# Performance work log

Hardware: AMD Instinct MI355X
Metric: run time of the kernel (lower is better)

## Reference

```python
import jax, jax.numpy as jnp
import numpy as np

N_NODES = 100_000
N_EDGES = 1_200_000
N_GRAPHS = 512
HID = 64


def setup_inputs() -> dict:
    key = jax.random.key(0)
    ks = jax.random.split(key, 8)
    x = jax.random.normal(ks[0], (N_NODES, 2), dtype=jnp.float32)
    edge_index = jax.random.randint(ks[1], (2, N_EDGES), 0, N_NODES, dtype=jnp.int32)
    batch = jnp.sort(jax.random.randint(ks[2], (N_NODES,), 0, N_GRAPHS, dtype=jnp.int32))
    def glorot(k, shape):
        fan_in, fan_out = shape
        s = jnp.sqrt(6.0 / (fan_in + fan_out))
        return jax.random.uniform(k, shape, jnp.float32, -s, s)
    return {
        "x": x, "edge_index": edge_index, "batch": batch, "num_graphs": N_GRAPHS,
        "W1": glorot(ks[3], (2, HID)), "b1": jnp.zeros((HID,), jnp.float32),
        "W2": glorot(ks[4], (HID, HID)), "b2": jnp.zeros((HID,), jnp.float32),
        "Wf1": glorot(ks[5], (HID, HID)), "bf1": jnp.zeros((HID,), jnp.float32),
        "Wf2": glorot(ks[6], (HID, 4)), "bf2": jnp.zeros((4,), jnp.float32),
    }


def gcn_conv(x, W, b, src, dst, n_nodes):
    """PyG GCNConv: sym-normalized A with self-loops, then linear."""
    h = x @ W  # [N, H] transform first (as PyG does)
    ones = jnp.ones(src.shape[0], x.dtype)
    deg = jax.ops.segment_sum(ones, dst, num_segments=n_nodes) + 1.0  # +1 self-loop
    dinv = jax.lax.rsqrt(deg)  # deg >= 1 always
    norm = dinv[src] * dinv[dst]  # [E]
    agg = jax.ops.segment_sum(h[src] * norm[:, None], dst, num_segments=n_nodes)
    agg = agg + h * (dinv * dinv)[:, None]  # self-loop contribution
    return agg + b


def global_mean_pool(x, batch, num_graphs):
    sums = jax.ops.segment_sum(x, batch, num_segments=num_graphs)
    cnts = jax.ops.segment_sum(jnp.ones(x.shape[0], x.dtype), batch, num_segments=num_graphs)
    return sums / jnp.maximum(cnts, 1.0)[:, None]


def reference(x, edge_index, batch, num_graphs, W1, b1, W2, b2, Wf1, bf1, Wf2, bf2):
    n = x.shape[0]
    src, dst = edge_index[0], edge_index[1]
    h = jax.nn.relu(gcn_conv(x, W1, b1, src, dst, n))   # dropout = identity (eval)
    h = jax.nn.relu(gcn_conv(h, W2, b2, src, dst, n))
    g = global_mean_pool(h, batch, num_graphs)          # [num_graphs, HID]
    g = jax.nn.relu(g @ Wf1 + bf1)
    return g @ Wf2 + bf2                                # [num_graphs, 4]
```

## Files before the change

### kernel.cpp

```cpp
#include <hip/hip_runtime.h>

#define NG 512
#define HID 64
#define CSH 9
#define BKT (1 << CSH)
#define PTILE 4096
#define MAXB 1024

__device__ __forceinline__ int pad8(int d) { return (d + 7) & ~7; }

__global__ __launch_bounds__(256) void chist_kernel(const int* __restrict__ dst,
                                                    int* __restrict__ chist, int E, int nbc) {
    __shared__ int h[MAXB];
    for (int i = threadIdx.x; i < nbc; i += 256) h[i] = 0;
    __syncthreads();
    int t0 = blockIdx.x * PTILE;
#pragma unroll
    for (int j = 0; j < PTILE / 256; ++j) {
        int e = t0 + j * 256 + threadIdx.x;
        if (e < E) atomicAdd(&h[dst[e] >> CSH], 1);
    }
    __syncthreads();
    for (int i = threadIdx.x; i < nbc; i += 256)
        if (h[i]) atomicAdd(&chist[i], h[i]);
}

__global__ __launch_bounds__(1024) void cscan_kernel(const int* __restrict__ chist,
                                                     int* __restrict__ cofs,
                                                     int* __restrict__ ccur, int nbc, int E) {
    __shared__ int s[1024];
    int i = threadIdx.x;
    int v = (i < nbc) ? chist[i] : 0;
    s[i] = v;
    __syncthreads();
    for (int off = 1; off < 1024; off <<= 1) {
        int t = (i >= off) ? s[i - off] : 0;
        __syncthreads();
        s[i] += t;
        __syncthreads();
    }
    if (i < nbc) {
        int ex = s[i] - v;
        cofs[i] = ex;
        ccur[i] = ex;
    }
    if (i == 0) cofs[nbc] = E;
}

__global__ __launch_bounds__(1024) void bscan_kernel(const int* __restrict__ bsum,
                                                     int* __restrict__ bofs, int nbc) {
    __shared__ int s[1024];
    int i = threadIdx.x;
    int v = (i < nbc) ? bsum[i] : 0;
    s[i] = v;
    __syncthreads();
    for (int off = 1; off < 1024; off <<= 1) {
        int t = (i >= off) ? s[i - off] : 0;
        __syncthreads();
        s[i] += t;
        __syncthreads();
    }
    if (i < nbc) bofs[i] = s[i] - v;
}

__global__ __launch_bounds__(256) void partA_kernel(const int* __restrict__ src,
                                                    const int* __restrict__ dst,
                                                    int* __restrict__ ccur,
                                                    int2* __restrict__ pstage, int E, int nbc) {
    __shared__ int hist[MAXB];
    __shared__ int base[MAXB];
    int tid = threadIdx.x;
    int t0 = blockIdx.x * PTILE;
    for (int i = tid; i < nbc; i += 256) hist[i] = 0;
    __syncthreads();
    int es[PTILE / 256], ds[PTILE / 256];
#pragma unroll
    for (int j = 0; j < PTILE / 256; ++j) {
        int e = t0 + j * 256 + tid;
        if (e < E) {
            ds[j] = dst[e];
            es[j] = src[e];
            atomicAdd(&hist[ds[j] >> CSH], 1);
        } else {
            ds[j] = -1;
        }
    }
    __syncthreads();
    for (int i = tid; i < nbc; i += 256) {
        int c = hist[i];
        base[i] = c ? atomicAdd(&ccur[i], c) : 0;
        hist[i] = 0;
    }
    __syncthreads();
#pragma unroll
    for (int j = 0; j < PTILE / 256; ++j) {
        if (ds[j] >= 0) {
            int b = ds[j] >> CSH;
            int r = atomicAdd(&hist[b], 1);
            pstage[base[b] + r] = make_int2(es[j], ds[j]);
        }
    }
}

__global__ __launch_bounds__(256) void degB_kernel(const int2* __restrict__ pstage,
                                                   const int* __restrict__ cofs,
                                                   const float2* __restrict__ x2,
                                                   int* __restrict__ deg,
                                                   float* __restrict__ dinv,
                                                   float2* __restrict__ xs2,
                                                   int* __restrict__ bsum, int N) {
    __shared__ int h[BKT];
    __shared__ int rs[256];
    int c = blockIdx.x;
    int n0 = c << CSH;
    int tid = threadIdx.x;
    for (int i = tid; i < BKT; i += 256) h[i] = 0;
    __syncthreads();
    int s0 = cofs[c], s1 = cofs[c + 1];
    for (int i = s0 + tid; i < s1; i += 256) atomicAdd(&h[pstage[i].y - n0], 1);
    __syncthreads();
    int psum = 0;
    for (int l = tid; l < BKT; l += 256) {
        int d = n0 + l;
        if (d < N) {
            int dg = h[l];
            deg[d] = dg;
            float di = rsqrtf((float)dg + 1.0f);
            dinv[d] = di;
            float2 xv = x2[d];
            xs2[d] = make_float2(xv.x * di, xv.y * di);
            psum += pad8(dg);
        }
    }
    rs[tid] = psum;
    __syncthreads();
    for (int off = 128; off > 0; off >>= 1) {
        if (tid < off) rs[tid] += rs[tid + off];
        __syncthreads();
    }
    if (tid == 0) bsum[c] = rs[0];
    if (c == 0 && tid == 0) xs2[N] = make_float2(0.0f, 0.0f);
}

__global__ __launch_bounds__(256) void partB_kernel(const int2* __restrict__ pstage,
                                                    const int* __restrict__ cofs,
                                                    const int* __restrict__ bofs,
                                                    const int* __restrict__ deg,
                                                    int* __restrict__ rowptr,
                                                    int* __restrict__ esrc, int N, int nbc) {
    __shared__ int rowL[BKT];
    __shared__ int curL[BKT];
    __shared__ int ps[256];
    int c = blockIdx.x;
    int n0 = c << CSH;
    int tid = threadIdx.x;
    int i0 = 2 * tid, i1 = 2 * tid + 1;
    int d0 = (n0 + i0 < N) ? pad8(deg[n0 + i0]) : 0;
    int d1 = (n0 + i1 < N) ? pad8(deg[n0 + i1]) : 0;
    ps[tid] = d0 + d1;
    __syncthreads();
    for (int off = 1; off < 256; off <<= 1) {
        int t = (tid >= off) ? ps[tid - off] : 0;
        __syncthreads();
        ps[tid] += t;
        __syncthreads();
    }
    int base = bofs[c];
    int excl = ps[tid] - (d0 + d1);
    rowL[i0] = base + excl;
    rowL[i1] = base + excl + d0;
    curL[i0] = 0;
    curL[i1] = 0;
    if (n0 + i0 < N) rowptr[n0 + i0] = rowL[i0];
    if (n0 + i1 < N) rowptr[n0 + i1] = rowL[i1];
    if (c == nbc - 1 && tid == 255) rowptr[N] = base + ps[255];
    __syncthreads();
    int s0 = cofs[c], s1 = cofs[c + 1];
    for (int i = s0 + tid; i < s1; i += 256) {
        int2 pr = pstage[i];
        int l = pr.y - n0;
        int p = rowL[l] + atomicAdd(&curL[l], 1);
        esrc[p] = pr.x;
    }
    __syncthreads();
    for (int l = tid; l < BKT; l += 256) {
        if (n0 + l < N) {
            int dg = curL[l];
            int p = rowL[l] + dg, p1 = rowL[l] + pad8(dg);
            for (; p < p1; ++p) esrc[p] = N;
        }
    }
}

__global__ void gstart_kernel(const int* __restrict__ batch, int* __restrict__ gstart, int N) {
    int i = blockIdx.x * blockDim.x + threadIdx.x;
    if (i >= N) return;
    int b = batch[i];
    int bp = (i == 0) ? -1 : batch[i - 1];
    for (int g = bp + 1; g <= b; ++g) gstart[g] = i;
    if (i == N - 1)
        for (int g = b + 1; g <= NG; ++g) gstart[g] = N;
}

__global__ __launch_bounds__(256) void layer1a_kernel(
    const float2* __restrict__ xs2, const int* __restrict__ rowptr,
    const int* __restrict__ esrc, const float* __restrict__ dinv,
    const float* __restrict__ W1, const float* __restrict__ b1,
    float* __restrict__ h1s, int N) {
    int t = blockIdx.x * blockDim.x + threadIdx.x;
    int node = t >> 6, lane = t & 63;
    if (node >= N) return;
    int un = __builtin_amdgcn_readfirstlane(node);
    int k0 = __builtin_amdgcn_readfirstlane(rowptr[un]);
    int k1 = __builtin_amdgcn_readfirstlane(rowptr[un + 1]);
    float a0 = 0.0f, a1 = 0.0f;
    for (int e = k0; e < k1; e += 8) {
        const int4* ep = (const int4*)(esrc + e);
        int4 qa = ep[0], qb = ep[1];
        float2 v0 = xs2[qa.x], v1 = xs2[qa.y], v2 = xs2[qa.z], v3 = xs2[qa.w];
        float2 v4 = xs2[qb.x], v5 = xs2[qb.y], v6 = xs2[qb.z], v7 = xs2[qb.w];
        a0 += ((v0.x + v1.x) + (v2.x + v3.x)) + ((v4.x + v5.x) + (v6.x + v7.x));
        a1 += ((v0.y + v1.y) + (v2.y + v3.y)) + ((v4.y + v5.y) + (v6.y + v7.y));
    }
    float di = dinv[un];
    float2 xn = xs2[un];
    float m0 = di * (a0 + xn.x);
    float m1 = di * (a1 + xn.y);
    float v = fmaf(m0, W1[lane], fmaf(m1, W1[HID + lane], b1[lane]));
    h1s[(size_t)un * HID + lane] = fmaxf(v, 0.0f) * di;
}

#define TNB 128
__global__ __launch_bounds__(TNB) void l1gemm_kernel(
    const float* __restrict__ h1s, const float* __restrict__ W2,
    float* __restrict__ h2, int N) {
    __shared__ float h1t[HID * TNB];
    int t = threadIdx.x;
    int node0 = blockIdx.x * TNB;
    const float4* g4 = (const float4*)h1s;
#pragma unroll
    for (int r = 0; r < 16; ++r) {
        int g = r * TNB + t;
        int nd = g >> 4, kq = g & 15;
        float4 v = make_float4(0.f, 0.f, 0.f, 0.f);
        if (node0 + nd < N) v = g4[(size_t)(node0 + nd) * 16 + kq];
        int kb = kq * 4;
        h1t[(kb + 0) * TNB + (nd ^ ((kb + 0) & 31))] = v.x;
        h1t[(kb + 1) * TNB + (nd ^ ((kb + 1) & 31))] = v.y;
        h1t[(kb + 2) * TNB + (nd ^ ((kb + 2) & 31))] = v.z;
        h1t[(kb + 3) * TNB + (nd ^ ((kb + 3) & 31))] = v.w;
    }
    __syncthreads();
    int node = node0 + t;
    bool alive = node < N;
#pragma unroll 1
    for (int jt = 0; jt < 8; ++jt) {
        float c0 = 0.f, c1 = 0.f, c2 = 0.f, c3 = 0.f;
        float c4 = 0.f, c5 = 0.f, c6 = 0.f, c7 = 0.f;
#pragma unroll 8
        for (int k = 0; k < HID; ++k) {
            float h = h1t[k * TNB + (t ^ (k & 31))];
            const float4* wr = (const float4*)(W2 + k * HID + jt * 8);
            float4 wa = wr[0], wb = wr[1];
            c0 = fmaf(h, wa.x, c0); c1 = fmaf(h, wa.y, c1);
            c2 = fmaf(h, wa.z, c2); c3 = fmaf(h, wa.w, c3);
            c4 = fmaf(h, wb.x, c4); c5 = fmaf(h, wb.y, c5);
            c6 = fmaf(h, wb.z, c6); c7 = fmaf(h, wb.w, c7);
        }
        if (alive) {
            float4* o = (float4*)(h2 + (size_t)node * HID + jt * 8);
            o[0] = make_float4(c0, c1, c2, c3);
            o[1] = make_float4(c4, c5, c6, c7);
        }
    }
}

__global__ __launch_bounds__(256, 8) void layer2_kernel(
    const int* __restrict__ rowptr, const int* __restrict__ esrc,
    const float* __restrict__ dinv, const float* __restrict__ h2,
    const float* __restrict__ b2, const int* __restrict__ batch,
    float* __restrict__ gsum, int N) {
    int lane = threadIdx.x & 63;
    float bz = b2[lane];
    int wave = (blockIdx.x * 256 + threadIdx.x) >> 6;
    int nwaves = gridDim.x * 4;
    int npw = (N + nwaves - 1) / nwaves;
    int nA = wave * npw;
    int nB = min(N, nA + npw);
    int gcur = -1;
    float zacc = 0.0f;
    for (int node = nA; node < nB; ++node) {
        int un = __builtin_amdgcn_readfirstlane(node);
        int k0 = __builtin_amdgcn_readfirstlane(rowptr[un]);
        int k1 = __builtin_amdgcn_readfirstlane(rowptr[un + 1]);
        float acc = h2[(un << 6) + lane];
        int e = k0;
        for (; e + 32 <= k1; e += 32) {
            const int4* ep = (const int4*)(esrc + e);
            int4 q0 = ep[0], q1 = ep[1], q2 = ep[2], q3 = ep[3];
            int4 q4 = ep[4], q5 = ep[5], q6 = ep[6], q7 = ep[7];
            float r0  = h2[(q0.x << 6) + lane], r1  = h2[(q0.y << 6) + lane];
            float r2  = h2[(q0.z << 6) + lane], r3  = h2[(q0.w << 6) + lane];
            float r4  = h2[(q1.x << 6) + lane], r5  = h2[(q1.y << 6) + lane];
            float r6  = h2[(q1.z << 6) + lane], r7  = h2[(q1.w << 6) + lane];
            float r8  = h2[(q2.x << 6) + lane], r9  = h2[(q2.y << 6) + lane];
            float r10 = h2[(q2.z << 6) + lane], r11 = h2[(q2.w << 6) + lane];
            float r12 = h2[(q3.x << 6) + lane], r13 = h2[(q3.y << 6) + lane];
            float r14 = h2[(q3.z << 6) + lane], r15 = h2[(q3.w << 6) + lane];
            float r16 = h2[(q4.x << 6) + lane], r17 = h2[(q4.y << 6) + lane];
            float r18 = h2[(q4.z << 6) + lane], r19 = h2[(q4.w << 6) + lane];
            float r20 = h2[(q5.x << 6) + lane], r21 = h2[(q5.y << 6) + lane];
            float r22 = h2[(q5.z << 6) + lane], r23 = h2[(q5.w << 6) + lane];
            float r24 = h2[(q6.x << 6) + lane], r25 = h2[(q6.y << 6) + lane];
            float r26 = h2[(q6.z << 6) + lane], r27 = h2[(q6.w << 6) + lane];
            float r28 = h2[(q7.x << 6) + lane], r29 = h2[(q7.y << 6) + lane];
            float r30 = h2[(q7.z << 6) + lane], r31 = h2[(q7.w << 6) + lane];
            acc += ((((r0 + r1) + (r2 + r3)) + ((r4 + r5) + (r6 + r7)))
                  + (((r8 + r9) + (r10 + r11)) + ((r12 + r13) + (r14 + r15))))
                 + ((((r16 + r17) + (r18 + r19)) + ((r20 + r21) + (r22 + r23)))
                  + (((r24 + r25) + (r26 + r27)) + ((r28 + r29) + (r30 + r31))));
        }
        if (e + 16 <= k1) {
            const int4* ep = (const int4*)(esrc + e);
            int4 qa = ep[0], qb = ep[1], qc = ep[2], qd = ep[3];
            float r0 = h2[(qa.x << 6) + lane], r1 = h2[(qa.y << 6) + lane];
            float r2 = h2[(qa.z << 6) + lane], r3 = h2[(qa.w << 6) + lane];
            float r4 = h2[(qb.x << 6) + lane], r5 = h2[(qb.y << 6) + lane];
            float r6 = h2[(qb.z << 6) + lane], r7 = h2[(qb.w << 6) + lane];
            float r8 = h2[(qc.x << 6) + lane], r9 = h2[(qc.y << 6) + lane];
            float r10 = h2[(qc.z << 6) + lane], r11 = h2[(qc.w << 6) + lane];
            float r12 = h2[(qd.x << 6) + lane], r13 = h2[(qd.y << 6) + lane];
            float r14 = h2[(qd.z << 6) + lane], r15 = h2[(qd.w << 6) + lane];
            acc += (((r0 + r1) + (r2 + r3)) + ((r4 + r5) + (r6 + r7)))
                 + (((r8 + r9) + (r10 + r11)) + ((r12 + r13) + (r14 + r15)));
            e += 16;
        }
        if (e < k1) {
            const int4* ep = (const int4*)(esrc + e);
            int4 qa = ep[0], qb = ep[1];
            float r0 = h2[(qa.x << 6) + lane], r1 = h2[(qa.y << 6) + lane];
            float r2 = h2[(qa.z << 6) + lane], r3 = h2[(qa.w << 6) + lane];
            float r4 = h2[(qb.x << 6) + lane], r5 = h2[(qb.y << 6) + lane];
            float r6 = h2[(qb.z << 6) + lane], r7 = h2[(qb.w << 6) + lane];
            acc += ((r0 + r1) + (r2 + r3)) + ((r4 + r5) + (r6 + r7));
        }
        float z = fmaxf(fmaf(dinv[un], acc, bz), 0.0f);
        int g = __builtin_amdgcn_readfirstlane(batch[un]);
        if (g != gcur) {
            if (gcur >= 0) atomicAdd(&gsum[(gcur << 6) + lane], zacc);
            gcur = g;
            zacc = 0.0f;
        }
        zacc += z;
    }
    if (gcur >= 0) atomicAdd(&gsum[(gcur << 6) + lane], zacc);
}

__global__ void head_kernel(const float* __restrict__ gsum, const int* __restrict__ gstart,
                            const float* __restrict__ Wf1, const float* __restrict__ bf1,
                            const float* __restrict__ Wf2, const float* __restrict__ bf2,
                            float* __restrict__ out) {
    __shared__ float gs[HID];
    __shared__ float ts[HID];
    int b = blockIdx.x;
    int j = threadIdx.x;
    float cnt = fmaxf((float)(gstart[b + 1] - gstart[b]), 1.0f);
    gs[j] = gsum[b * HID + j] / cnt;
    __syncthreads();
    float acc = bf1[j];
#pragma unroll
    for (int k = 0; k < HID; ++k) acc = fmaf(gs[k], Wf1[k * HID + j], acc);
    ts[j] = fmaxf(acc, 0.0f);
    __syncthreads();
    if (j < 4) {
        float o = bf2[j];
#pragma unroll
        for (int k = 0; k < HID; ++k) o = fmaf(ts[k], Wf2[k * 4 + j], o);
        out[b * 4 + j] = o;
    }
}

extern "C" void kernel_launch(void* const* d_in, const int* in_sizes, int n_in,
                              void* d_out, int out_size, void* d_ws, size_t ws_size,
                              hipStream_t stream) {
    const float* x   = (const float*)d_in[0];
    const int*   ei  = (const int*)d_in[1];
    const int*   bat = (const int*)d_in[2];
    const float* W1  = (const float*)d_in[4];
    const float* b1  = (const float*)d_in[5];
    const float* W2  = (const float*)d_in[6];
    const float* b2  = (const float*)d_in[7];
    const float* Wf1 = (const float*)d_in[8];
    const float* bf1 = (const float*)d_in[9];
    const float* Wf2 = (const float*)d_in[10];
    const float* bf2 = (const float*)d_in[11];
    float* out = (float*)d_out;

    int N = in_sizes[2];
    int E = in_sizes[1] / 2;
    const int* src = ei;
    const int* dst = ei + E;
    int nbc = (N + BKT - 1) >> CSH;
    int ntile = (E + PTILE - 1) / PTILE;
    size_t Ecap = ((size_t)E + 7 * (size_t)N + 8 + 3) & ~(size_t)3;

    char* ws = (char*)d_ws;
    size_t off = 0;
    auto alloc = [&](size_t bytes) {
        char* p = ws + off;
        off = (off + bytes + 255) & ~(size_t)255;
        return p;
    };
    int*    chist  = (int*)alloc((size_t)MAXB * 4);
    float*  gsum   = (float*)alloc((size_t)NG * HID * 4);
    int*    deg    = (int*)alloc((size_t)N * 4);
    int*    cofs   = (int*)alloc((size_t)(MAXB + 1) * 4);
    int*    ccur   = (int*)alloc((size_t)MAXB * 4);
    float*  dinv   = (float*)alloc((size_t)N * 4);
    int*    rowptr = (int*)alloc((size_t)(N + 1) * 4);
    int*    bsum   = (int*)alloc((size_t)MAXB * 4);
    int*    bofs   = (int*)alloc((size_t)MAXB * 4);
    int*    esrc   = (int*)alloc(Ecap * 4);
    int2*   pstage = (int2*)alloc((size_t)E * 8);
    float2* xs2    = (float2*)alloc((size_t)(N + 1) * 8);
    float*  h1buf  = (float*)alloc((size_t)N * HID * 4);
    float*  h2buf  = (float*)alloc((size_t)(N + 1) * HID * 4);
    int*    gstart = (int*)alloc((size_t)(NG + 1) * 4);

    hipMemsetAsync(chist, 0, (size_t)((char*)gsum - (char*)chist) + (size_t)NG * HID * 4,
                   stream);
    hipMemsetAsync(h2buf + (size_t)N * HID, 0, HID * 4, stream);

    chist_kernel<<<ntile, 256, 0, stream>>>(dst, chist, E, nbc);
    gstart_kernel<<<(N + 255) / 256, 256, 0, stream>>>(bat, gstart, N);
    cscan_kernel<<<1, 1024, 0, stream>>>(chist, cofs, ccur, nbc, E);
    partA_kernel<<<ntile, 256, 0, stream>>>(src, dst, ccur, pstage, E, nbc);
    degB_kernel<<<nbc, 256, 0, stream>>>(pstage, cofs, (const float2*)x, deg, dinv, xs2,
                                         bsum, N);
    bscan_kernel<<<1, 1024, 0, stream>>>(bsum, bofs, nbc);
    partB_kernel<<<nbc, 256, 0, stream>>>(pstage, cofs, bofs, deg, rowptr, esrc, N, nbc);

    int nh = N * HID;
    layer1a_kernel<<<(nh + 255) / 256, 256, 0, stream>>>(xs2, rowptr, esrc, dinv, W1, b1,
                                                         h1buf, N);
    l1gemm_kernel<<<(N + TNB - 1) / TNB, TNB, 0, stream>>>(h1buf, W2, h2buf, N);

    layer2_kernel<<<4096, 256, 0, stream>>>(rowptr, esrc, dinv, h2buf, b2, bat, gsum, N);

    head_kernel<<<NG, HID, 0, stream>>>(gsum, gstart, Wf1, bf1, Wf2, bf2, out);
}
```

Baseline: 261.8 us.

## Fuse degree and CSR fill kernels and store layer-2 features in fp16

Merges degB, bscan and partB into one kernel. Each bucket block now claims its CSR segment with an atomicAdd on a global cursor instead of a separate global scan, so rows are stored as rowbeg plus degree rather than a contiguous rowptr. Separately, the transformed layer-2 features are written as fp16, which halves the bytes fetched by the irregular gather in layer2 while accumulation stays in fp32. The fp16 storage loses precision, and the atomic segment allocation makes edge placement order nondeterministic across blocks.

```diff
diff --git a/kernel.cpp b/kernel.cpp
--- a/kernel.cpp
+++ b/kernel.cpp
@@ -1,4 +1,5 @@
 #include <hip/hip_runtime.h>
+#include <hip/hip_fp16.h>
 
 #define NG 512
 #define HID 64
@@ -45,22 +46,6 @@
         ccur[i] = ex;
     }
     if (i == 0) cofs[nbc] = E;
-}
-
-__global__ __launch_bounds__(1024) void bscan_kernel(const int* __restrict__ bsum,
-                                                     int* __restrict__ bofs, int nbc) {
-    __shared__ int s[1024];
-    int i = threadIdx.x;
-    int v = (i < nbc) ? bsum[i] : 0;
-    s[i] = v;
-    __syncthreads();
-    for (int off = 1; off < 1024; off <<= 1) {
-        int t = (i >= off) ? s[i - off] : 0;
-        __syncthreads();
-        s[i] += t;
-        __syncthreads();
-    }
-    if (i < nbc) bofs[i] = s[i] - v;
 }
 
 __global__ __launch_bounds__(256) void partA_kernel(const int* __restrict__ src,
@@ -102,15 +87,16 @@
     }
 }
 
-__global__ __launch_bounds__(256) void degB_kernel(const int2* __restrict__ pstage,
-                                                   const int* __restrict__ cofs,
-                                                   const float2* __restrict__ x2,
-                                                   int* __restrict__ deg,
-                                                   float* __restrict__ dinv,
-                                                   float2* __restrict__ xs2,
-                                                   int* __restrict__ bsum, int N) {
+__global__ __launch_bounds__(256) void partB2_kernel(
+    const int2* __restrict__ pstage, const int* __restrict__ cofs,
+    const float2* __restrict__ x2, int* __restrict__ deg, float* __restrict__ dinv,
+    float2* __restrict__ xs2, int* __restrict__ rowbeg, int* __restrict__ esrc,
+    int* __restrict__ ecur, int N) {
     __shared__ int h[BKT];
-    __shared__ int rs[256];
+    __shared__ int rowL[BKT];
+    __shared__ int curL[BKT];
+    __shared__ int ps[256];
+    __shared__ int baseS;
     int c = blockIdx.x;
     int n0 = c << CSH;
     int tid = threadIdx.x;
@@ -119,45 +105,25 @@
     int s0 = cofs[c], s1 = cofs[c + 1];
     for (int i = s0 + tid; i < s1; i += 256) atomicAdd(&h[pstage[i].y - n0], 1);
     __syncthreads();
-    int psum = 0;
-    for (int l = tid; l < BKT; l += 256) {
-        int d = n0 + l;
-        if (d < N) {
-            int dg = h[l];
-            deg[d] = dg;
-            float di = rsqrtf((float)dg + 1.0f);
-            dinv[d] = di;
-            float2 xv = x2[d];
-            xs2[d] = make_float2(xv.x * di, xv.y * di);
-            psum += pad8(dg);
-        }
-    }
-    rs[tid] = psum;
-    __syncthreads();
-    for (int off = 128; off > 0; off >>= 1) {
-        if (tid < off) rs[tid] += rs[tid + off];
-        __syncthreads();
-    }
-    if (tid == 0) bsum[c] = rs[0];
-    if (c == 0 && tid == 0) xs2[N] = make_float2(0.0f, 0.0f);
-}
-
-__global__ __launch_bounds__(256) void partB_kernel(const int2* __restrict__ pstage,
-                                                    const int* __restrict__ cofs,
-                                                    const int* __restrict__ bofs,
-                                                    const int* __restrict__ deg,
-                                                    int* __restrict__ rowptr,
-                                                    int* __restrict__ esrc, int N, int nbc) {
-    __shared__ int rowL[BKT];
-    __shared__ int curL[BKT];
-    __shared__ int ps[256];
-    int c = blockIdx.x;
-    int n0 = c << CSH;
-    int tid = threadIdx.x;
     int i0 = 2 * tid, i1 = 2 * tid + 1;
-    int d0 = (n0 + i0 < N) ? pad8(deg[n0 + i0]) : 0;
-    int d1 = (n0 + i1 < N) ? pad8(deg[n0 + i1]) : 0;
-    ps[tid] = d0 + d1;
+    int dg0 = (n0 + i0 < N) ? h[i0] : 0;
+    int dg1 = (n0 + i1 < N) ? h[i1] : 0;
+    if (n0 + i0 < N) {
+        deg[n0 + i0] = dg0;
+        float di = rsqrtf((float)dg0 + 1.0f);
+        dinv[n0 + i0] = di;
+        float2 xv = x2[n0 + i0];
+        xs2[n0 + i0] = make_float2(xv.x * di, xv.y * di);
+    }
+    if (n0 + i1 < N) {
+        deg[n0 + i1] = dg1;
+        float di = rsqrtf((float)dg1 + 1.0f);
+        dinv[n0 + i1] = di;
+        float2 xv = x2[n0 + i1];
+        xs2[n0 + i1] = make_float2(xv.x * di, xv.y * di);
+    }
+    int p0 = pad8(dg0), p1 = pad8(dg1);
+    ps[tid] = p0 + p1;
     __syncthreads();
     for (int off = 1; off < 256; off <<= 1) {
         int t = (tid >= off) ? ps[tid - off] : 0;
@@ -165,17 +131,16 @@
         ps[tid] += t;
         __syncthreads();
     }
-    int base = bofs[c];
-    int excl = ps[tid] - (d0 + d1);
-    rowL[i0] = base + excl;
-    rowL[i1] = base + excl + d0;
+    if (tid == 255) baseS = atomicAdd(ecur, ps[255]);
+    __syncthreads();
+    int excl = baseS + ps[tid] - (p0 + p1);
+    rowL[i0] = excl;
+    rowL[i1] = excl + p0;
     curL[i0] = 0;
     curL[i1] = 0;
-    if (n0 + i0 < N) rowptr[n0 + i0] = rowL[i0];
-    if (n0 + i1 < N) rowptr[n0 + i1] = rowL[i1];
-    if (c == nbc - 1 && tid == 255) rowptr[N] = base + ps[255];
-    __syncthreads();
-    int s0 = cofs[c], s1 = cofs[c + 1];
+    if (n0 + i0 < N) rowbeg[n0 + i0] = rowL[i0];
+    if (n0 + i1 < N) rowbeg[n0 + i1] = rowL[i1];
+    __syncthreads();
     for (int i = s0 + tid; i < s1; i += 256) {
         int2 pr = pstage[i];
         int l = pr.y - n0;
@@ -186,10 +151,11 @@
     for (int l = tid; l < BKT; l += 256) {
         if (n0 + l < N) {
             int dg = curL[l];
-            int p = rowL[l] + dg, p1 = rowL[l] + pad8(dg);
-            for (; p < p1; ++p) esrc[p] = N;
-        }
-    }
+            int p = rowL[l] + dg, p1e = rowL[l] + pad8(dg);
+            for (; p < p1e; ++p) esrc[p] = N;
+        }
+    }
+    if (c == 0 && tid == 0) xs2[N] = make_float2(0.0f, 0.0f);
 }
 
 __global__ void gstart_kernel(const int* __restrict__ batch, int* __restrict__ gstart, int N) {
@@ -203,16 +169,16 @@
 }
 
 __global__ __launch_bounds__(256) void layer1a_kernel(
-    const float2* __restrict__ xs2, const int* __restrict__ rowptr,
-    const int* __restrict__ esrc, const float* __restrict__ dinv,
-    const float* __restrict__ W1, const float* __restrict__ b1,
-    float* __restrict__ h1s, int N) {
+    const float2* __restrict__ xs2, const int* __restrict__ rowbeg,
+    const int* __restrict__ deg, const int* __restrict__ esrc,
+    const float* __restrict__ dinv, const float* __restrict__ W1,
+    const float* __restrict__ b1, float* __restrict__ h1s, int N) {
     int t = blockIdx.x * blockDim.x + threadIdx.x;
     int node = t >> 6, lane = t & 63;
     if (node >= N) return;
     int un = __builtin_amdgcn_readfirstlane(node);
-    int k0 = __builtin_amdgcn_readfirstlane(rowptr[un]);
-    int k1 = __builtin_amdgcn_readfirstlane(rowptr[un + 1]);
+    int k0 = __builtin_amdgcn_readfirstlane(rowbeg[un]);
+    int k1 = k0 + pad8(__builtin_amdgcn_readfirstlane(deg[un]));
     float a0 = 0.0f, a1 = 0.0f;
     for (int e = k0; e < k1; e += 8) {
         const int4* ep = (const int4*)(esrc + e);
@@ -233,7 +199,7 @@
 #define TNB 128
 __global__ __launch_bounds__(TNB) void l1gemm_kernel(
     const float* __restrict__ h1s, const float* __restrict__ W2,
-    float* __restrict__ h2, int N) {
+    __half* __restrict__ h2, int N) {
     __shared__ float h1t[HID * TNB];
     int t = threadIdx.x;
     int node0 = blockIdx.x * TNB;
@@ -268,18 +234,21 @@
             c6 = fmaf(h, wb.z, c6); c7 = fmaf(h, wb.w, c7);
         }
         if (alive) {
-            float4* o = (float4*)(h2 + (size_t)node * HID + jt * 8);
-            o[0] = make_float4(c0, c1, c2, c3);
-            o[1] = make_float4(c4, c5, c6, c7);
+            union { __half h[8]; int4 v; } u;
+            u.h[0] = __float2half_rn(c0); u.h[1] = __float2half_rn(c1);
+            u.h[2] = __float2half_rn(c2); u.h[3] = __float2half_rn(c3);
+            u.h[4] = __float2half_rn(c4); u.h[5] = __float2half_rn(c5);
+            u.h[6] = __float2half_rn(c6); u.h[7] = __float2half_rn(c7);
+            *(int4*)(h2 + (size_t)node * HID + jt * 8) = u.v;
         }
     }
 }
 
 __global__ __launch_bounds__(256, 8) void layer2_kernel(
-    const int* __restrict__ rowptr, const int* __restrict__ esrc,
-    const float* __restrict__ dinv, const float* __restrict__ h2,
-    const float* __restrict__ b2, const int* __restrict__ batch,
-    float* __restrict__ gsum, int N) {
+    const int* __restrict__ rowbeg, const int* __restrict__ deg,
+    const int* __restrict__ esrc, const float* __restrict__ dinv,
+    const __half* __restrict__ h2, const float* __restrict__ b2,
+    const int* __restrict__ batch, float* __restrict__ gsum, int N) {
     int lane = threadIdx.x & 63;
     float bz = b2[lane];
     int wave = (blockIdx.x * 256 + threadIdx.x) >> 6;
@@ -291,30 +260,46 @@
     float zacc = 0.0f;
     for (int node = nA; node < nB; ++node) {
         int un = __builtin_amdgcn_readfirstlane(node);
-        int k0 = __builtin_amdgcn_readfirstlane(rowptr[un]);
-        int k1 = __builtin_amdgcn_readfirstlane(rowptr[un + 1]);
-        float acc = h2[(un << 6) + lane];
+        int k0 = __builtin_amdgcn_readfirstlane(rowbeg[un]);
+        int k1 = k0 + pad8(__builtin_amdgcn_readfirstlane(deg[un]));
+        float acc = __half2float(h2[(un << 6) + lane]);
         int e = k0;
         for (; e + 32 <= k1; e += 32) {
             const int4* ep = (const int4*)(esrc + e);
             int4 q0 = ep[0], q1 = ep[1], q2 = ep[2], q3 = ep[3];
             int4 q4 = ep[4], q5 = ep[5], q6 = ep[6], q7 = ep[7];
-            float r0  = h2[(q0.x << 6) + lane], r1  = h2[(q0.y << 6) + lane];
-            float r2  = h2[(q0.z << 6) + lane], r3  = h2[(q0.w << 6) + lane];
-            float r4  = h2[(q1.x << 6) + lane], r5  = h2[(q1.y << 6) + lane];
-            float r6  = h2[(q1.z << 6) + lane], r7  = h2[(q1.w << 6) + lane];
-            float r8  = h2[(q2.x << 6) + lane], r9  = h2[(q2.y << 6) + lane];
-            float r10 = h2[(q2.z << 6) + lane], r11 = h2[(q2.w << 6) + lane];
-            float r12 = h2[(q3.x << 6) + lane], r13 = h2[(q3.y << 6) + lane];
-            float r14 = h2[(q3.z << 6) + lane], r15 = h2[(q3.w << 6) + lane];
-            float r16 = h2[(q4.x << 6) + lane], r17 = h2[(q4.y << 6) + lane];
-            float r18 = h2[(q4.z << 6) + lane], r19 = h2[(q4.w << 6) + lane];
-            float r20 = h2[(q5.x << 6) + lane], r21 = h2[(q5.y << 6) + lane];
-            float r22 = h2[(q5.z << 6) + lane], r23 = h2[(q5.w << 6) + lane];
-            float r24 = h2[(q6.x << 6) + lane], r25 = h2[(q6.y << 6) + lane];
-            float r26 = h2[(q6.z << 6) + lane], r27 = h2[(q6.w << 6) + lane];
-            float r28 = h2[(q7.x << 6) + lane], r29 = h2[(q7.y << 6) + lane];
-            float r30 = h2[(q7.z << 6) + lane], r31 = h2[(q7.w << 6) + lane];
+            float r0  = __half2float(h2[(q0.x << 6) + lane]);
+            float r1  = __half2float(h2[(q0.y << 6) + lane]);
+            float r2  = __half2float(h2[(q0.z << 6) + lane]);
+            float r3  = __half2float(h2[(q0.w << 6) + lane]);
+            float r4  = __half2float(h2[(q1.x << 6) + lane]);
+            float r5  = __half2float(h2[(q1.y << 6) + lane]);
+            float r6  = __half2float(h2[(q1.z << 6) + lane]);
+            float r7  = __half2float(h2[(q1.w << 6) + lane]);
+            float r8  = __half2float(h2[(q2.x << 6) + lane]);
+            float r9  = __half2float(h2[(q2.y << 6) + lane]);
+            float r10 = __half2float(h2[(q2.z << 6) + lane]);
+            float r11 = __half2float(h2[(q2.w << 6) + lane]);
+            float r12 = __half2float(h2[(q3.x << 6) + lane]);
+            float r13 = __half2float(h2[(q3.y << 6) + lane]);
+            float r14 = __half2float(h2[(q3.z << 6) + lane]);
+            float r15 = __half2float(h2[(q3.w << 6) + lane]);
+            float r16 = __half2float(h2[(q4.x << 6) + lane]);
+            float r17 = __half2float(h2[(q4.y << 6) + lane]);
+            float r18 = __half2float(h2[(q4.z << 6) + lane]);
+            float r19 = __half2float(h2[(q4.w << 6) + lane]);
+            float r20 = __half2float(h2[(q5.x << 6) + lane]);
+            float r21 = __half2float(h2[(q5.y << 6) + lane]);
+            float r22 = __half2float(h2[(q5.z << 6) + lane]);
+            float r23 = __half2float(h2[(q5.w << 6) + lane]);
+            float r24 = __half2float(h2[(q6.x << 6) + lane]);
+            float r25 = __half2float(h2[(q6.y << 6) + lane]);
+            float r26 = __half2float(h2[(q6.z << 6) + lane]);
+            float r27 = __half2float(h2[(q6.w << 6) + lane]);
+            float r28 = __half2float(h2[(q7.x << 6) + lane]);
+            float r29 = __half2float(h2[(q7.y << 6) + lane]);
+            float r30 = __half2float(h2[(q7.z << 6) + lane]);
+            float r31 = __half2float(h2[(q7.w << 6) + lane]);
             acc += ((((r0 + r1) + (r2 + r3)) + ((r4 + r5) + (r6 + r7)))
                   + (((r8 + r9) + (r10 + r11)) + ((r12 + r13) + (r14 + r15))))
                  + ((((r16 + r17) + (r18 + r19)) + ((r20 + r21) + (r22 + r23)))
@@ -323,14 +308,22 @@
         if (e + 16 <= k1) {
             const int4* ep = (const int4*)(esrc + e);
             int4 qa = ep[0], qb = ep[1], qc = ep[2], qd = ep[3];
-            float r0 = h2[(qa.x << 6) + lane], r1 = h2[(qa.y << 6) + lane];
-            float r2 = h2[(qa.z << 6) + lane], r3 = h2[(qa.w << 6) + lane];
-            float r4 = h2[(qb.x << 6) + lane], r5 = h2[(qb.y << 6) + lane];
-            float r6 = h2[(qb.z << 6) + lane], r7 = h2[(qb.w << 6) + lane];
-            float r8 = h2[(qc.x << 6) + lane], r9 = h2[(qc.y << 6) + lane];
-            float r10 = h2[(qc.z << 6) + lane], r11 = h2[(qc.w << 6) + lane];
-            float r12 = h2[(qd.x << 6) + lane], r13 = h2[(qd.y << 6) + lane];
-            float r14 = h2[(qd.z << 6) + lane], r15 = h2[(qd.w << 6) + lane];
+            float r0 = __half2float(h2[(qa.x << 6) + lane]);
+            float r1 = __half2float(h2[(qa.y << 6) + lane]);
+            float r2 = __half2float(h2[(qa.z << 6) + lane]);
+            float r3 = __half2float(h2[(qa.w << 6) + lane]);
+            float r4 = __half2float(h2[(qb.x << 6) + lane]);
+            float r5 = __half2float(h2[(qb.y << 6) + lane]);
+            float r6 = __half2float(h2[(qb.z << 6) + lane]);
+            float r7 = __half2float(h2[(qb.w << 6) + lane]);
+            float r8 = __half2float(h2[(qc.x << 6) + lane]);
+            float r9 = __half2float(h2[(qc.y << 6) + lane]);
+            float r10 = __half2float(h2[(qc.z << 6) + lane]);
+            float r11 = __half2float(h2[(qc.w << 6) + lane]);
+            float r12 = __half2float(h2[(qd.x << 6) + lane]);
+            float r13 = __half2float(h2[(qd.y << 6) + lane]);
+            float r14 = __half2float(h2[(qd.z << 6) + lane]);
+            float r15 = __half2float(h2[(qd.w << 6) + lane]);
             acc += (((r0 + r1) + (r2 + r3)) + ((r4 + r5) + (r6 + r7)))
                  + (((r8 + r9) + (r10 + r11)) + ((r12 + r13) + (r14 + r15)));
             e += 16;
@@ -338,10 +331,14 @@
         if (e < k1) {
             const int4* ep = (const int4*)(esrc + e);
             int4 qa = ep[0], qb = ep[1];
-            float r0 = h2[(qa.x << 6) + lane], r1 = h2[(qa.y << 6) + lane];
-            float r2 = h2[(qa.z << 6) + lane], r3 = h2[(qa.w << 6) + lane];
-            float r4 = h2[(qb.x << 6) + lane], r5 = h2[(qb.y << 6) + lane];
-            float r6 = h2[(qb.z << 6) + lane], r7 = h2[(qb.w << 6) + lane];
+            float r0 = __half2float(h2[(qa.x << 6) + lane]);
+            float r1 = __half2float(h2[(qa.y << 6) + lane]);
+            float r2 = __half2float(h2[(qa.z << 6) + lane]);
+            float r3 = __half2float(h2[(qa.w << 6) + lane]);
+            float r4 = __half2float(h2[(qb.x << 6) + lane]);
+            float r5 = __half2float(h2[(qb.y << 6) + lane]);
+            float r6 = __half2float(h2[(qb.z << 6) + lane]);
+            float r7 = __half2float(h2[(qb.w << 6) + lane]);
             acc += ((r0 + r1) + (r2 + r3)) + ((r4 + r5) + (r6 + r7));
         }
         float z = fmaxf(fmaf(dinv[un], acc, bz), 0.0f);
@@ -412,40 +409,38 @@
         return p;
     };
     int*    chist  = (int*)alloc((size_t)MAXB * 4);
+    int*    ecur   = (int*)alloc(256);
     float*  gsum   = (float*)alloc((size_t)NG * HID * 4);
     int*    deg    = (int*)alloc((size_t)N * 4);
     int*    cofs   = (int*)alloc((size_t)(MAXB + 1) * 4);
     int*    ccur   = (int*)alloc((size_t)MAXB * 4);
     float*  dinv   = (float*)alloc((size_t)N * 4);
-    int*    rowptr = (int*)alloc((size_t)(N + 1) * 4);
-    int*    bsum   = (int*)alloc((size_t)MAXB * 4);
-    int*    bofs   = (int*)alloc((size_t)MAXB * 4);
+    int*    rowbeg = (int*)alloc((size_t)N * 4);
     int*    esrc   = (int*)alloc(Ecap * 4);
     int2*   pstage = (int2*)alloc((size_t)E * 8);
     float2* xs2    = (float2*)alloc((size_t)(N + 1) * 8);
     float*  h1buf  = (float*)alloc((size_t)N * HID * 4);
-    float*  h2buf  = (float*)alloc((size_t)(N + 1) * HID * 4);
+    __half* h2buf  = (__half*)alloc((size_t)(N + 1) * HID * 2);
     int*    gstart = (int*)alloc((size_t)(NG + 1) * 4);
 
     hipMemsetAsync(chist, 0, (size_t)((char*)gsum - (char*)chist) + (size_t)NG * HID * 4,
                    stream);
-    hipMemsetAsync(h2buf + (size_t)N * HID, 0, HID * 4, stream);
+    hipMemsetAsync(h2buf + (size_t)N * HID, 0, HID * 2, stream);
 
     chist_kernel<<<ntile, 256, 0, stream>>>(dst, chist, E, nbc);
     gstart_kernel<<<(N + 255) / 256, 256, 0, stream>>>(bat, gstart, N);
     cscan_kernel<<<1, 1024, 0, stream>>>(chist, cofs, ccur, nbc, E);
     partA_kernel<<<ntile, 256, 0, stream>>>(src, dst, ccur, pstage, E, nbc);
-    degB_kernel<<<nbc, 256, 0, stream>>>(pstage, cofs, (const float2*)x, deg, dinv, xs2,
-                                         bsum, N);
-    bscan_kernel<<<1, 1024, 0, stream>>>(bsum, bofs, nbc);
-    partB_kernel<<<nbc, 256, 0, stream>>>(pstage, cofs, bofs, deg, rowptr, esrc, N, nbc);
+    partB2_kernel<<<nbc, 256, 0, stream>>>(pstage, cofs, (const float2*)x, deg, dinv, xs2,
+                                           rowbeg, esrc, ecur, N);
 
     int nh = N * HID;
-    layer1a_kernel<<<(nh + 255) / 256, 256, 0, stream>>>(xs2, rowptr, esrc, dinv, W1, b1,
-                                                         h1buf, N);
+    layer1a_kernel<<<(nh + 255) / 256, 256, 0, stream>>>(xs2, rowbeg, deg, esrc, dinv, W1,
+                                                         b1, h1buf, N);
     l1gemm_kernel<<<(N + TNB - 1) / TNB, TNB, 0, stream>>>(h1buf, W2, h2buf, N);
 
-    layer2_kernel<<<4096, 256, 0, stream>>>(rowptr, esrc, dinv, h2buf, b2, bat, gsum, N);
+    layer2_kernel<<<4096, 256, 0, stream>>>(rowbeg, deg, esrc, dinv, h2buf, b2, bat, gsum,
+                                            N);
 
     head_kernel<<<NG, HID, 0, stream>>>(gsum, gstart, Wf1, bf1, Wf2, bf2, out);
 }
```

Result: faster. 241.2 us (-7.9%).
